# Kernel optimization log

Hardware: AMD Instinct MI355X
Metric: run time of the kernel (lower is better)

## Reference

```python
import jax, jax.numpy as jnp
import numpy as np

B, S, D, H = 4, 1024, 1024, 16
HD = D // H


def setup_inputs() -> dict:
    key = jax.random.key(0)
    ks = jax.random.split(key, 12)
    s = 1.0 / np.sqrt(D)
    inp = {
        'q': jax.random.normal(ks[0], (B, S, D), jnp.float32),
        'k': jax.random.normal(ks[1], (B, S, D), jnp.float32),
        'v': jax.random.normal(ks[2], (B, S, D), jnp.float32),
        'mask': jnp.broadcast_to(jnp.tril(jnp.ones((S, S), jnp.int32)), (B, S, S)),
        'Wq': jax.random.uniform(ks[3], (D, D), jnp.float32, -s, s),
        'bq': jax.random.uniform(ks[4], (D,), jnp.float32, -s, s),
        'Wk': jax.random.uniform(ks[5], (D, D), jnp.float32, -s, s),
        'bk': jax.random.uniform(ks[6], (D,), jnp.float32, -s, s),
        'Wv': jax.random.uniform(ks[7], (D, D), jnp.float32, -s, s),
        'bv': jax.random.uniform(ks[8], (D,), jnp.float32, -s, s),
        'Wo': jax.random.uniform(ks[9], (D, D), jnp.float32, -s, s),
        'bo': jax.random.uniform(ks[10], (D,), jnp.float32, -s, s),
    }
    return inp


def _split_heads(x):
    # [B,S,D] -> [B,H,S,HD]
    b, s, d = x.shape
    return x.reshape(b, s, H, HD).transpose(0, 2, 1, 3)


def reference(q, k, v, mask, Wq, bq, Wk, bk, Wv, bv, Wo, bo):
    # Linear projections (torch Linear: x @ W.T + b) followed by relu
    qh = jax.nn.relu(q @ Wq.T + bq)
    kh = jax.nn.relu(k @ Wk.T + bk)
    vh = jax.nn.relu(v @ Wv.T + bv)
    qh, kh, vh = _split_heads(qh), _split_heads(kh), _split_heads(vh)
    scores = jnp.einsum('bhqd,bhkd->bhqk', qh, kh) / jnp.sqrt(jnp.float32(HD))
    scores = jnp.where(mask[:, None, :, :] == 0, jnp.float32(-1e9), scores)
    attn = jax.nn.softmax(scores, axis=-1)
    y = jnp.einsum('bhqk,bhkd->bhqd', attn, vh)
    y = y.transpose(0, 2, 1, 3).reshape(B, S, D)  # merge heads
    return jax.nn.relu(y @ Wo.T + bo)
```

## Files before the change

### kernel.cpp

```cpp
#include <hip/hip_runtime.h>


using f16    = _Float16;
using f16x4  = __attribute__((ext_vector_type(4))) _Float16;
using f16x8  = __attribute__((ext_vector_type(8))) _Float16;
using f32x4  = __attribute__((ext_vector_type(4))) float;
using f32x16 = __attribute__((ext_vector_type(16))) float;

static constexpr int S = 1024, Dm = 1024, NH = 16, HD = 64;

#if __has_builtin(__builtin_amdgcn_mfma_f32_32x32x16_f16)
#define USE_G32 1
#define MFMA32(ACC, A_, B_) \
    (ACC) = __builtin_amdgcn_mfma_f32_32x32x16_f16((A_), (B_), (ACC), 0, 0, 0)
#else
#define USE_G32 0
#endif

#if __has_builtin(__builtin_amdgcn_mfma_f32_16x16x32_f16) && \
    __has_builtin(__builtin_amdgcn_mfma_f32_16x16x16f16)
#define USE_A16 1
#define MFMA16K32(ACC, A_, B_) \
    (ACC) = __builtin_amdgcn_mfma_f32_16x16x32_f16((A_), (B_), (ACC), 0, 0, 0)
#define MFMA16(ACC, A_, B_) \
    (ACC) = __builtin_amdgcn_mfma_f32_16x16x16f16((A_), (B_), (ACC), 0, 0, 0)
#else
#define USE_A16 0
#endif

#define LO4(v) __builtin_shufflevector((v), (v), 0, 1, 2, 3)
#define HI4(v) __builtin_shufflevector((v), (v), 4, 5, 6, 7)

__device__ __forceinline__ f16x4 cvt4(float4 a) {
    f16x4 r; r[0] = (f16)a.x; r[1] = (f16)a.y; r[2] = (f16)a.z; r[3] = (f16)a.w;
    return r;
}

__device__ __forceinline__ int pcol64(int k) {
#if USE_A16
    return ((k >> 3) & 3) * 16 + ((k >> 5) << 3) + (k & 7);
#else
    return ((k >> 2) & 3) * 16 + ((k >> 4) << 2) + (k & 3);
#endif
}

__device__ __forceinline__ int swz(int row, int col) {
    return (col & ~31) | ((((col >> 3) ^ (row >> 1)) & 3) << 3) | (col & 7);
}

__device__ __forceinline__ void store_out(void* out, int mode, int m, int n, float v) {
    const int b_ = m >> 10, s_ = m & 1023, h_ = n >> 6, hd_ = n & 63;
    const size_t idx = (mode == 0)
        ? (((size_t)(b_ * NH + h_) * S + s_) * HD + pcol64(hd_))
        : (((size_t)(b_ * NH + h_) * HD + hd_) * S + s_);
    ((f16*)out)[idx] = (f16)v;
}

#if __has_builtin(__builtin_amdgcn_global_load_lds)
#define HAS_GLL 1
#else
#define HAS_GLL 0
#endif

__device__ __forceinline__ void gll16(const void* g, void* l) {
#if HAS_GLL
    __builtin_amdgcn_global_load_lds(
        (const __attribute__((address_space(1))) void*)g,
        (__attribute__((address_space(3))) void*)l, 16, 0, 0);
#else
    *(uint4*)l = *(const uint4*)g;
#endif
}

__global__ __launch_bounds__(256)
void cvt_w(const float* __restrict__ s0, const float* __restrict__ s1,
           const float* __restrict__ s2, f16* __restrict__ dst)
{
    const int z = blockIdx.y;
    const float* src = (z == 0) ? s0 : (z == 1) ? s1 : s2;
    const int e = blockIdx.x * 256 + threadIdx.x;
    const int n = e >> 8;
    const int k = (e & 255) * 4;
    const float4 v = *(const float4*)(src + (size_t)n * Dm + k);
    *(f16x4*)(dst + (size_t)z * Dm * Dm + (size_t)n * Dm + swz(n, k)) = cvt4(v);
}

__global__ __launch_bounds__(512, 6)
void gemm_qkv(const float* __restrict__ q, const float* __restrict__ k,
              const float* __restrict__ v, const f16* __restrict__ wqkv,
              const float* __restrict__ bq, const float* __restrict__ bk,
              const float* __restrict__ bv,
              f16* __restrict__ qh, f16* __restrict__ kh, f16* __restrict__ vt)
{
    const int z = blockIdx.z;
    const float* A = (z == 0) ? q : (z == 1) ? k : v;
    const float* bias = (z == 0) ? bq : (z == 1) ? bk : bv;
    f16* out = (z == 0) ? qh : (z == 1) ? kh : vt;
    const int mode = (z == 2) ? 1 : 0;
    const f16* Wf = wqkv + (size_t)z * Dm * Dm;

    const int tid = threadIdx.x;
    const int bm = blockIdx.x, bn = blockIdx.y;
#if USE_G32
    __shared__ alignas(16) float As[2][128][32];
    __shared__ alignas(16) f16   Ws[2][128][32];

    const int lane = tid & 63, wave = tid >> 6;
    const int l31 = lane & 31, kh2 = lane >> 5;
    const int wm = wave & 3, wn = wave >> 2;

    const int arow = tid >> 3;
    const int aslotD = tid & 7;
    const int aslotS = aslotD ^ (arow & 7);
    const float* Asrc0 = A + (size_t)(bm * 128 + arow) * Dm + aslotS * 4;
    const int wrow = tid >> 2, wcol = (tid & 3) * 8;
    const f16* Wsrc0 = Wf + (size_t)(bn * 128 + wrow) * Dm + wcol;

    auto dma = [&](int k0, int buf) {
        gll16(Asrc0 + k0,                      &As[buf][arow][aslotD * 4]);
        gll16(Asrc0 + (size_t)64 * Dm + k0,    &As[buf][64 + arow][aslotD * 4]);
        gll16(Wsrc0 + k0,                      &Ws[buf][wrow][wcol]);
    };

    auto afrag = [&](int buf, int r, int s) -> f16x8 {
        const int p = s * 4 + kh2 * 2, r7 = r & 7;
        const f32x4 lo = *(const f32x4*)&As[buf][r][(p ^ r7) * 4];
        const f32x4 hi = *(const f32x4*)&As[buf][r][((p + 1) ^ r7) * 4];
        f16x8 f;
        f[0] = (f16)lo[0]; f[1] = (f16)lo[1]; f[2] = (f16)lo[2]; f[3] = (f16)lo[3];
        f[4] = (f16)hi[0]; f[5] = (f16)hi[1]; f[6] = (f16)hi[2]; f[7] = (f16)hi[3];
        return f;
    };
    auto wfrag = [&](int buf, int r, int s) -> f16x8 {
        const int sl = s * 2 + kh2;
        return *(const f16x8*)&Ws[buf][r][((sl ^ (r >> 1)) & 3) * 8];
    };

    f32x16 acc[2] = {};
    auto kslice = [&](int buf, int s) {
        const f16x8 af  = afrag(buf, wm * 32 + l31, s);
        const f16x8 bf0 = wfrag(buf, wn * 64 + l31, s);
        const f16x8 bf1 = wfrag(buf, wn * 64 + 32 + l31, s);
        MFMA32(acc[0], af, bf0);
        MFMA32(acc[1], af, bf1);
    };

    constexpr int NIT = Dm / 32;
    dma(0, 0);
    for (int t = 0; t < NIT; ++t) {
        const int cur = t & 1;
        __syncthreads();
        if (t + 1 < NIT) dma((t + 1) * 32, cur ^ 1);
        kslice(cur, 0);
        kslice(cur, 1);
    }

#pragma unroll
    for (int j = 0; j < 2; ++j) {
        const int col = bn * 128 + wn * 64 + j * 32 + l31;
        const float bb = bias[col];
#pragma unroll
        for (int blk = 0; blk < 4; ++blk) {
            const int row0 = bm * 128 + wm * 32 + 8 * blk + 4 * kh2;
            if (mode == 1) {
                const int b_ = row0 >> 10, s_ = row0 & 1023;
                const int h_ = col >> 6, hd_ = col & 63;
                f16x4 vv;
#pragma unroll
                for (int r = 0; r < 4; ++r)
                    vv[r] = (f16)fmaxf(acc[j][blk * 4 + r] + bb, 0.0f);
                *(f16x4*)&out[((size_t)(b_ * NH + h_) * HD + hd_) * S + s_] = vv;
            } else {
#pragma unroll
                for (int r = 0; r < 4; ++r)
                    store_out(out, mode, row0 + r, col,
                              fmaxf(acc[j][blk * 4 + r] + bb, 0.0f));
            }
        }
    }
#else
    for (int i = tid; i < 128 * 128; i += 512) {
        const int m = bm * 128 + (i >> 7);
        const int n = bn * 128 + (i & 127);
        float acc = 0.0f;
        for (int k2 = 0; k2 < Dm; ++k2)
            acc = fmaf(A[(size_t)m * Dm + k2], (float)Wf[(size_t)n * Dm + swz(n, k2)], acc);
        store_out(out, mode, m, n, fmaxf(acc + bias[n], 0.0f));
    }
#endif
}

__global__ __launch_bounds__(256, 6)
void gemm_out(const f16* __restrict__ y, const float* __restrict__ wo,
              const float* __restrict__ bo, float* __restrict__ out)
{
    const int tid = threadIdx.x;
    const int bm = blockIdx.x, bn = blockIdx.y;
#if USE_G32
    __shared__ alignas(16) f16   As[2][64][32];
    __shared__ alignas(16) float Wsf[2][64][32];

    const int lane = tid & 63, wave = tid >> 6;
    const int l31 = lane & 31, kh2 = lane >> 5;
    const int wm = wave & 1, wn = wave >> 1;

    const int drow = tid >> 2, dcol = (tid & 3) * 8;
    const f16* Asrc = y + (size_t)(bm * 64 + drow) * Dm + dcol;
    const int wrow = tid >> 3;
    const int wslotD = tid & 7;
    const int wslotS = wslotD ^ (wrow & 7);
    const float* Wsrc0 = wo + (size_t)(bn * 64 + wrow) * Dm + wslotS * 4;

    auto dma = [&](int k0, int buf) {
        gll16(Asrc + k0, &As[buf][drow][dcol]);
        gll16(Wsrc0 + k0,                   &Wsf[buf][wrow][wslotD * 4]);
        gll16(Wsrc0 + (size_t)32 * Dm + k0, &Wsf[buf][32 + wrow][wslotD * 4]);
    };
    auto yfrag = [&](int buf, int r, int s) -> f16x8 {
        const int sl = s * 2 + kh2;
        return *(const f16x8*)&As[buf][r][((sl ^ (r >> 1)) & 3) * 8];
    };
    auto wfrag32 = [&](int buf, int r, int s) -> f16x8 {
        const int p = s * 4 + kh2 * 2, r7 = r & 7;
        const f32x4 lo = *(const f32x4*)&Wsf[buf][r][(p ^ r7) * 4];
        const f32x4 hi = *(const f32x4*)&Wsf[buf][r][((p + 1) ^ r7) * 4];
        f16x8 f;
        f[0] = (f16)lo[0]; f[1] = (f16)lo[1]; f[2] = (f16)lo[2]; f[3] = (f16)lo[3];
        f[4] = (f16)hi[0]; f[5] = (f16)hi[1]; f[6] = (f16)hi[2]; f[7] = (f16)hi[3];
        return f;
    };

    f32x16 acc = {};
    constexpr int NIT = Dm / 32;
    dma(0, 0);
    for (int t = 0; t < NIT; ++t) {
        const int cur = t & 1;
        __syncthreads();
        if (t + 1 < NIT) dma((t + 1) * 32, cur ^ 1);
#pragma unroll
        for (int s = 0; s < 2; ++s) {
            const f16x8 af = yfrag(cur, wm * 32 + l31, s);
            const f16x8 bf = wfrag32(cur, wn * 32 + l31, s);
            MFMA32(acc, af, bf);
        }
    }

    const int col = bn * 64 + wn * 32 + l31;
    const float bb = bo[col];
#pragma unroll
    for (int blk = 0; blk < 4; ++blk) {
        const int row0 = bm * 64 + wm * 32 + 8 * blk + 4 * kh2;
#pragma unroll
        for (int r = 0; r < 4; ++r)
            out[(size_t)(row0 + r) * Dm + col] = fmaxf(acc[blk * 4 + r] + bb, 0.0f);
    }
#else
    for (int i = tid; i < 64 * 64; i += 256) {
        const int m = bm * 64 + (i >> 6);
        const int n = bn * 64 + (i & 63);
        float acc = 0.0f;
        for (int k2 = 0; k2 < Dm; ++k2)
            acc = fmaf((float)y[(size_t)m * Dm + swz(m, k2)],
                       wo[(size_t)n * Dm + k2], acc);
        out[(size_t)m * Dm + n] = fmaxf(acc + bo[n], 0.0f);
    }
#endif
}

__global__ __launch_bounds__(512, 6)
void attn_fwd(const f16* __restrict__ qh, const f16* __restrict__ kh,
              const f16* __restrict__ vt, f16* __restrict__ y)
{
    const int bz = blockIdx.x;
    const int hid = (bz & 7) * 8 + ((bz >> 3) & 7);
    const int qt  = bz >> 6;
    const int h   = hid & 15;
    const int b   = hid >> 4;
    const size_t head = (size_t)(b * NH + h) * S * HD;

#if USE_A16
    __shared__ alignas(16) f16 Ks[2][64][72];
    __shared__ alignas(16) f16 Vs[2][64][72];

    const int tid  = threadIdx.x;
    const int wave = tid >> 6;
    const int lane = tid & 63;
    const int l15  = lane & 15;
    const int quad = lane >> 4;
    const int sr   = tid >> 3;
    const int t8   = tid & 7;

    const f16* Qrow = qh + head + (size_t)(qt * 128 + wave * 16 + l15) * HD;
    const f16* Kp   = kh + head;
    const f16* Vp   = vt + head;

    f16x8 aq[2];
    {
        const uint4 q0 = *(const uint4*)(Qrow + quad * 16);
        const uint4 q1 = *(const uint4*)(Qrow + quad * 16 + 8);
        aq[0] = *(f16x8*)&q0;
        aq[1] = *(f16x8*)&q1;
    }

    const int qg = qt * 128 + wave * 16 + l15;
    const int wave_qmax = qt * 128 + wave * 16 + 15;
    float m_i = -1e30f, l_i = 0.0f;
    f32x4 acc_o[4] = {};

    const int vc0 = 16 * ((2 * t8) & 3) + 4 * (t8 >> 1);
    const int vc1 = 16 * ((2 * t8 + 1) & 3) + 4 * (t8 >> 1);

    uint4 pk, pv;
    auto pref = [&](int kt) {
        pk = *(const uint4*)(Kp + (size_t)(kt * 64 + sr) * HD + t8 * 8);
        pv = *(const uint4*)(Vp + (size_t)sr * S + kt * 64 + t8 * 8);
    };

    const int ktmax = 2 * qt + 1;
    pref(0);
    for (int kt = 0; kt <= ktmax; ++kt) {
        const int cur = kt & 1;
        *(uint4*)&Ks[cur][sr][t8 * 8] = pk;
        {
            f16x8 pv8 = *(f16x8*)&pv;
            *(f16x4*)&Vs[cur][sr][vc0] = LO4(pv8);
            *(f16x4*)&Vs[cur][sr][vc1] = HI4(pv8);
        }
        __syncthreads();
        if (kt < ktmax) pref(kt + 1);

        if (kt * 64 <= wave_qmax) {
            f32x4 accs[4] = {};
#pragma unroll
            for (int t = 0; t < 4; ++t) {
                const f16x8 k8a = *(const f16x8*)&Ks[cur][t * 16 + l15][quad * 16];
                const f16x8 k8b = *(const f16x8*)&Ks[cur][t * 16 + l15][quad * 16 + 8];
                MFMA16K32(accs[t], k8a, aq[0]);
                MFMA16K32(accs[t], k8b, aq[1]);
            }

            const int key0 = kt * 64 + quad * 4;
#pragma unroll
            for (int t = 0; t < 4; ++t)
#pragma unroll
                for (int r = 0; r < 4; ++r) {
                    float sv = accs[t][r] * 0.125f;
                    if (key0 + t * 16 + r > qg) sv = -1e9f;
                    accs[t][r] = sv;
                }

            float mx = accs[0][0];
#pragma unroll
            for (int t = 0; t < 4; ++t)
#pragma unroll
                for (int r = 0; r < 4; ++r) mx = fmaxf(mx, accs[t][r]);
            mx = fmaxf(mx, __shfl_xor(mx, 16, 64));
            mx = fmaxf(mx, __shfl_xor(mx, 32, 64));
            const float mnew = fmaxf(m_i, mx);
            float sm = 0.0f;
#pragma unroll
            for (int t = 0; t < 4; ++t)
#pragma unroll
                for (int r = 0; r < 4; ++r) {
                    const float e = __expf(accs[t][r] - mnew);
                    accs[t][r] = e;
                    sm += e;
                }
            sm += __shfl_xor(sm, 16, 64);
            sm += __shfl_xor(sm, 32, 64);
            const float alpha = __expf(m_i - mnew);
            l_i = l_i * alpha + sm;
            m_i = mnew;

            f16x4 ap[4];
#pragma unroll
            for (int c = 0; c < 4; ++c) {
                f16x4 v;
#pragma unroll
                for (int j = 0; j < 4; ++j) v[j] = (f16)accs[c][j];
                ap[c] = v;
            }

            float ar[4];
#pragma unroll
            for (int r = 0; r < 4; ++r) ar[r] = __shfl(alpha, quad * 4 + r, 64);
#pragma unroll
            for (int t2 = 0; t2 < 4; ++t2)
#pragma unroll
                for (int r = 0; r < 4; ++r) acc_o[t2][r] *= ar[r];
#pragma unroll
            for (int t2 = 0; t2 < 4; ++t2) {
                const f16x8 v8a = *(const f16x8*)&Vs[cur][t2 * 16 + l15][quad * 16];
                const f16x8 v8b = *(const f16x8*)&Vs[cur][t2 * 16 + l15][quad * 16 + 8];
                MFMA16(acc_o[t2], ap[0], LO4(v8a));
                MFMA16(acc_o[t2], ap[1], HI4(v8a));
                MFMA16(acc_o[t2], ap[2], LO4(v8b));
                MFMA16(acc_o[t2], ap[3], HI4(v8b));
            }
        }
    }

    float lr[4];
#pragma unroll
    for (int r = 0; r < 4; ++r) lr[r] = __shfl(l_i, quad * 4 + r, 64);
#pragma unroll
    for (int t2 = 0; t2 < 4; ++t2)
#pragma unroll
        for (int r = 0; r < 4; ++r) {
            const int srow = qt * 128 + wave * 16 + quad * 4 + r;
            const int dcol = h * 64 + t2 * 16 + l15;
            y[((size_t)b * S + srow) * Dm + swz(srow, dcol)] =
                (f16)(acc_o[t2][r] / lr[r]);
        }
#else
    const int tid = threadIdx.x;
    if (tid < 128) {
        const int q = qt * 128 + tid;
        const f16* Qr = qh + head + (size_t)q * HD;
        float qv[64];
        for (int d = 0; d < 64; ++d) qv[d] = (float)Qr[pcol64(d)];
        float mx = -1e30f;
        for (int key = 0; key <= q; ++key) {
            const f16* Kr = kh + head + (size_t)key * HD;
            float s = 0.0f;
            for (int d = 0; d < 64; ++d) s = fmaf(qv[d], (float)Kr[pcol64(d)], s);
            mx = fmaxf(mx, s * 0.125f);
        }
        float o[64];
        for (int d = 0; d < 64; ++d) o[d] = 0.0f;
        float l = 0.0f;
        for (int key = 0; key <= q; ++key) {
            const f16* Kr = kh + head + (size_t)key * HD;
            float s = 0.0f;
            for (int d = 0; d < 64; ++d) s = fmaf(qv[d], (float)Kr[pcol64(d)], s);
            const float p = __expf(s * 0.125f - mx);
            l += p;
            for (int d = 0; d < 64; ++d)
                o[d] = fmaf(p, (float)vt[head + (size_t)d * S + key], o[d]);
        }
        for (int d = 0; d < 64; ++d)
            y[((size_t)b * S + q) * Dm + swz(q, h * 64 + d)] = (f16)(o[d] / l);
    }
#endif
}

extern "C" void kernel_launch(void* const* d_in, const int* in_sizes, int n_in,
                              void* d_out, int out_size, void* d_ws, size_t ws_size,
                              hipStream_t stream)
{
    f16* ws = (f16*)d_ws;
    const size_t SEG = (size_t)4 * 1024 * 1024;
    f16* qh   = ws;
    f16* kh   = ws + SEG;
    f16* vt   = ws + 2 * SEG;
    f16* wqkv = ws + 3 * SEG;
    f16* y    = ws + 3 * SEG;

    cvt_w<<<dim3(1024, 3), 256, 0, stream>>>(
        (const float*)d_in[4], (const float*)d_in[6], (const float*)d_in[8], wqkv);
    gemm_qkv<<<dim3(32, 8, 3), 512, 0, stream>>>(
        (const float*)d_in[0], (const float*)d_in[1], (const float*)d_in[2],
        wqkv,
        (const float*)d_in[5], (const float*)d_in[7], (const float*)d_in[9],
        qh, kh, vt);
    attn_fwd<<<dim3(4 * NH * (S / 128)), 512, 0, stream>>>(qh, kh, vt, y);
    gemm_out<<<dim3(64, 16), 256, 0, stream>>>(
        y, (const float*)d_in[10], (const float*)d_in[11], (float*)d_out);
}
```

Before: 241.5 us.

## Split K across wave pairs in output GEMM with LDS reduction

The output projection GEMM goes from 256 to 512 threads per block. Each half of the waves handles one 32-wide half of a 64-wide K tile, so the loop runs half as many iterations, and the partial accumulators are summed through LDS before the bias and ReLU epilogue. This is meant to cut the number of serialized sync-bounded K iterations and raise wave-level parallelism. In exchange it doubles the LDS footprint, adds a reduction step with extra barriers, and larger blocks may lower occupancy.

New measurement: 245.9 us. About the same (+1.8%).

```diff
diff --git a/kernel.cpp b/kernel.cpp
--- a/kernel.cpp
+++ b/kernel.cpp
@@ -190,40 +190,40 @@
 #endif
 }
 
-__global__ __launch_bounds__(256, 6)
+__global__ __launch_bounds__(512, 6)
 void gemm_out(const f16* __restrict__ y, const float* __restrict__ wo,
               const float* __restrict__ bo, float* __restrict__ out)
 {
     const int tid = threadIdx.x;
     const int bm = blockIdx.x, bn = blockIdx.y;
 #if USE_G32
-    __shared__ alignas(16) f16   As[2][64][32];
-    __shared__ alignas(16) float Wsf[2][64][32];
+    __shared__ alignas(16) f16   As[2][64][64];
+    __shared__ alignas(16) float Wsf[2][64][64];
 
     const int lane = tid & 63, wave = tid >> 6;
     const int l31 = lane & 31, kh2 = lane >> 5;
-    const int wm = wave & 1, wn = wave >> 1;
-
-    const int drow = tid >> 2, dcol = (tid & 3) * 8;
-    const f16* Asrc = y + (size_t)(bm * 64 + drow) * Dm + dcol;
-    const int wrow = tid >> 3;
-    const int wslotD = tid & 7;
-    const int wslotS = wslotD ^ (wrow & 7);
-    const float* Wsrc0 = wo + (size_t)(bn * 64 + wrow) * Dm + wslotS * 4;
+    const int wm = wave & 1, wn = (wave >> 1) & 1, wk = wave >> 2;
+
+    const int yrow = tid >> 3, ycol8 = tid & 7;
+    const f16* Ysrc = y + (size_t)(bm * 64 + yrow) * Dm + ycol8 * 8;
+    const int wrow16 = tid >> 4, wslotD = tid & 15;
+    const int wpan = wslotD >> 3, wsl = wslotD & 7;
+    const float* Wsrc = wo + (size_t)(bn * 64 + wrow16) * Dm
+                           + wpan * 32 + (wsl ^ (wrow16 & 7)) * 4;
 
     auto dma = [&](int k0, int buf) {
-        gll16(Asrc + k0, &As[buf][drow][dcol]);
-        gll16(Wsrc0 + k0,                   &Wsf[buf][wrow][wslotD * 4]);
-        gll16(Wsrc0 + (size_t)32 * Dm + k0, &Wsf[buf][32 + wrow][wslotD * 4]);
-    };
-    auto yfrag = [&](int buf, int r, int s) -> f16x8 {
+        gll16(Ysrc + k0, &As[buf][yrow][ycol8 * 8]);
+        gll16(Wsrc + k0,                   &Wsf[buf][wrow16][wslotD * 4]);
+        gll16(Wsrc + (size_t)32 * Dm + k0, &Wsf[buf][32 + wrow16][wslotD * 4]);
+    };
+    auto yfrag = [&](int buf, int hp, int r, int s) -> f16x8 {
         const int sl = s * 2 + kh2;
-        return *(const f16x8*)&As[buf][r][((sl ^ (r >> 1)) & 3) * 8];
-    };
-    auto wfrag32 = [&](int buf, int r, int s) -> f16x8 {
+        return *(const f16x8*)&As[buf][r][hp * 32 + ((sl ^ (r >> 1)) & 3) * 8];
+    };
+    auto wfrag32 = [&](int buf, int hp, int r, int s) -> f16x8 {
         const int p = s * 4 + kh2 * 2, r7 = r & 7;
-        const f32x4 lo = *(const f32x4*)&Wsf[buf][r][(p ^ r7) * 4];
-        const f32x4 hi = *(const f32x4*)&Wsf[buf][r][((p + 1) ^ r7) * 4];
+        const f32x4 lo = *(const f32x4*)&Wsf[buf][r][hp * 32 + (p ^ r7) * 4];
+        const f32x4 hi = *(const f32x4*)&Wsf[buf][r][hp * 32 + (((p + 1) ^ r7) & 7) * 4];
         f16x8 f;
         f[0] = (f16)lo[0]; f[1] = (f16)lo[1]; f[2] = (f16)lo[2]; f[3] = (f16)lo[3];
         f[4] = (f16)hi[0]; f[5] = (f16)hi[1]; f[6] = (f16)hi[2]; f[7] = (f16)hi[3];
@@ -231,31 +231,46 @@
     };
 
     f32x16 acc = {};
-    constexpr int NIT = Dm / 32;
+    constexpr int NIT = Dm / 64;
     dma(0, 0);
     for (int t = 0; t < NIT; ++t) {
         const int cur = t & 1;
         __syncthreads();
-        if (t + 1 < NIT) dma((t + 1) * 32, cur ^ 1);
+        if (t + 1 < NIT) dma((t + 1) * 64, cur ^ 1);
 #pragma unroll
         for (int s = 0; s < 2; ++s) {
-            const f16x8 af = yfrag(cur, wm * 32 + l31, s);
-            const f16x8 bf = wfrag32(cur, wn * 32 + l31, s);
+            const f16x8 af = yfrag(cur, wk, wm * 32 + l31, s);
+            const f16x8 bf = wfrag32(cur, wk, wn * 32 + l31, s);
             MFMA32(acc, af, bf);
         }
     }
 
-    const int col = bn * 64 + wn * 32 + l31;
-    const float bb = bo[col];
-#pragma unroll
-    for (int blk = 0; blk < 4; ++blk) {
-        const int row0 = bm * 64 + wm * 32 + 8 * blk + 4 * kh2;
-#pragma unroll
-        for (int r = 0; r < 4; ++r)
-            out[(size_t)(row0 + r) * Dm + col] = fmaxf(acc[blk * 4 + r] + bb, 0.0f);
-    }
-#else
-    for (int i = tid; i < 64 * 64; i += 256) {
+    __syncthreads();
+    float* cb = (float*)&As[0][0][0];
+    const int region = (wm * 2 + wn) * 1024;
+    if (wk == 1) {
+#pragma unroll
+        for (int i = 0; i < 16; ++i)
+            cb[region + (8 * (i >> 2) + 4 * kh2 + (i & 3)) * 32 + l31] = acc[i];
+    }
+    __syncthreads();
+    if (wk == 0) {
+#pragma unroll
+        for (int i = 0; i < 16; ++i)
+            acc[i] += cb[region + (8 * (i >> 2) + 4 * kh2 + (i & 3)) * 32 + l31];
+
+        const int col = bn * 64 + wn * 32 + l31;
+        const float bb = bo[col];
+#pragma unroll
+        for (int blk = 0; blk < 4; ++blk) {
+            const int row0 = bm * 64 + wm * 32 + 8 * blk + 4 * kh2;
+#pragma unroll
+            for (int r = 0; r < 4; ++r)
+                out[(size_t)(row0 + r) * Dm + col] = fmaxf(acc[blk * 4 + r] + bb, 0.0f);
+        }
+    }
+#else
+    for (int i = tid; i < 64 * 64; i += 512) {
         const int m = bm * 64 + (i >> 6);
         const int n = bn * 64 + (i & 63);
         float acc = 0.0f;
@@ -464,6 +479,6 @@
         (const float*)d_in[5], (const float*)d_in[7], (const float*)d_in[9],
         qh, kh, vt);
     attn_fwd<<<dim3(4 * NH * (S / 128)), 512, 0, stream>>>(qh, kh, vt, y);
-    gemm_out<<<dim3(64, 16), 256, 0, stream>>>(
+    gemm_out<<<dim3(64, 16), 512, 0, stream>>>(
         y, (const float*)d_in[10], (const float*)d_in[11], (float*)d_out);
 }
```
